# Optimization experiments

Hardware: AMD Instinct MI355X
Metric: run time of the kernel (lower is better)

The kernel has to match this reference:

```python
import jax, jax.numpy as jnp
import numpy as np

EPS = 1e-5  # BatchNorm eps; eval mode with running_mean=0, running_var=1

def _bn(x, g, b):
    return x * (g / jnp.sqrt(1.0 + EPS)) + b

def _lrelu(x):
    return jnp.where(x >= 0, x, 0.2 * x)

def setup_inputs() -> dict:
    key = jax.random.key(0)
    ks = jax.random.split(key, 30)
    def w(i, shape, s=0.05):
        return jax.random.normal(ks[i], shape, dtype=jnp.float32) * s
    inp = {"x": jax.random.normal(ks[0], (8, 10, 4096), dtype=jnp.float32), "k": 20}
    inp.update(
        w1=w(1, (64, 9)),    g1=1.0 + w(2, (64,), 0.1),  b1=w(3, (64,), 0.1),
        w2=w(4, (64, 64)),   g2=1.0 + w(5, (64,), 0.1),  b2=w(6, (64,), 0.1),
        w3=w(7, (128, 128)), g3=1.0 + w(8, (128,), 0.1), b3=w(9, (128,), 0.1),
        w4=w(10, (256, 128)), g4=1.0 + w(11, (256,), 0.1), b4=w(12, (256,), 0.1),
        w5=w(13, (1024, 256)), g5=1.0 + w(14, (1024,), 0.1), b5=w(15, (1024,), 0.1),
        l1w=w(16, (512, 1472)), l1b=w(17, (512,), 0.1),
        g6=1.0 + w(18, (512,), 0.1), b6=w(19, (512,), 0.1),
        l2w=w(20, (256, 512)), l2b=w(21, (256,), 0.1),
        g7=1.0 + w(22, (256,), 0.1), b7=w(23, (256,), 0.1),
        l3w=w(24, (2, 256)), l3b=w(25, (2,), 0.1),
    )
    return inp

def reference(x, k, w1, g1, b1, w2, g2, b2, w3, g3, b3, w4, g4, b4, w5, g5, b5,
              l1w, l1b, g6, b6, l2w, l2b, g7, b7, l3w, l3b):
    B, C, N = x.shape
    # --- kNN on xyz (first 3 channels); topk of negative squared distance ---
    xyz = x[:, :3, :]
    xx = jnp.sum(xyz * xyz, axis=1)                        # [B,N]
    inner = jnp.einsum('bcn,bcm->bnm', xyz, xyz)           # [B,N,N]
    pd = 2.0 * inner - xx[:, :, None] - xx[:, None, :]     # -||xi-xj||^2
    idx = jax.lax.top_k(pd, k)[1]                          # [B,N,k]
    # --- neighbor gather + edge features (xyz_i, rgb_i, rgb_i - rgb_j) ---
    xt = jnp.transpose(x, (0, 2, 1))                       # [B,N,C]
    nbr = xt[jnp.arange(B)[:, None, None], idx]            # [B,N,k,C]
    xyz_i = jnp.broadcast_to(xt[:, :, None, :3], (B, N, k, 3))
    rgb_i = jnp.broadcast_to(xt[:, :, None, 3:6], (B, N, k, 3))
    f = jnp.concatenate([xyz_i, rgb_i, rgb_i - nbr[..., 3:6]], axis=-1)  # [B,N,k,9]
    # --- EdgeConv MLPs (1x1 convs) + max over neighbors ---
    h = _lrelu(_bn(jnp.einsum('bnkc,oc->bnko', f, w1), g1, b1))
    h = _lrelu(_bn(jnp.einsum('bnkc,oc->bnko', h, w2), g2, b2))
    x1 = jnp.max(h, axis=2)                                # [B,N,64]
    x2 = _lrelu(_bn(jnp.einsum('bnc,oc->bno', jnp.concatenate([x1, x1], -1), w3), g3, b3))  # [B,N,128]
    x3 = _lrelu(_bn(jnp.einsum('bnc,oc->bno', x2, w4), g4, b4))  # [B,N,256]
    x4 = jnp.max(x3, axis=1)                               # [B,256] global max pool
    # conv5 applied to x4 repeated over N; max over identical copies == itself
    xg = _lrelu(_bn(x4 @ w5.T, g5, b5))                    # [B,1024]
    feat = jnp.concatenate([jnp.broadcast_to(xg[:, None, :], (B, N, 1024)), x3, x2, x1], axis=-1)  # [B,N,1472]
    h = _lrelu(_bn(feat @ l1w.T + l1b, g6, b6))            # dropout = identity (eval)
    h = _lrelu(_bn(h @ l2w.T + l2b, g7, b7))
    out = h @ l3w.T + l3b                                  # [B,N,num_classes]
    return jnp.transpose(out, (0, 2, 1))                   # [B,num_classes,N]
```

## Files before the change

### kernel.cpp

```cpp
#include <hip/hip_runtime.h>


#define KNN 20
#define NPID 32768
#define RS 0.99999500003750f

#define X3_PO 8388608
#define X2_PO 4194304
#define X1_PO 2097152

typedef unsigned short ushort_t;
typedef unsigned int u32;
typedef __attribute__((ext_vector_type(8))) short bf16x8;
typedef __attribute__((ext_vector_type(4))) float f32x4;

#define LDS_PTR(p) ((__attribute__((address_space(3))) void*)(p))
#define GLB_PTR(p) ((const __attribute__((address_space(1))) void*)(p))

__device__ __forceinline__ float lrelu(float z) { return z >= 0.f ? z : 0.2f * z; }
__device__ __forceinline__ unsigned short f2bf(float f) {
  unsigned int u = __float_as_uint(f);
  return (unsigned short)((u + 0x7fffu + ((u >> 16) & 1u)) >> 16);
}
__device__ __forceinline__ float bf2f(unsigned short h) { return __uint_as_float((unsigned int)h << 16); }
__device__ __forceinline__ u32 pack2(u32 e0, u32 e1) { return (e1 << 16) | (e0 & 0xffffu); }
__device__ __forceinline__ u32 encf(float f) {
  const u32 u = __float_as_uint(f);
  return (u >> 31) ? ~u : (u | 0x80000000u);
}
__device__ __forceinline__ float decf(u32 e) {
  return __uint_as_float((e >> 31) ? (e ^ 0x80000000u) : ~e);
}
__device__ __forceinline__ f32x4 mfma16(uint4 a, uint4 b, f32x4 c) {
  return __builtin_amdgcn_mfma_f32_16x16x32_bf16(
      __builtin_bit_cast(bf16x8, a), __builtin_bit_cast(bf16x8, b), c, 0, 0, 0);
}

__global__ __launch_bounds__(256) void xyzw_kernel(const float* __restrict__ x, float4* __restrict__ xyzw) {
  const int i = blockIdx.x * 256 + threadIdx.x;
  const int b = i >> 12, n = i & 4095;
  const float* xb = x + (size_t)b * 40960;
  const float px = xb[n], py = xb[4096 + n], pz = xb[8192 + n];
  const float xx = __fadd_rn(__fadd_rn(__fmul_rn(px, px), __fmul_rn(py, py)), __fmul_rn(pz, pz));
  float4 v; v.x = px; v.y = py; v.z = pz; v.w = xx;
  xyzw[i] = v;
}

__global__ __launch_bounds__(1024) void knn_kernel(const float4* __restrict__ xyzw, int* __restrict__ idxo) {
  __shared__ __align__(16) float4 pt[4096];
  __shared__ float cval[16][64];
  __shared__ int cidx[16][64];
  const int tid = threadIdx.x, lane = tid & 63, wave = tid >> 6;
  const int pid = blockIdx.x * 16 + wave;
  const int b = pid >> 12, n = pid & 4095;
  const float4* xw = xyzw + ((size_t)b << 12);
#pragma unroll
  for (int r = 0; r < 4; ++r) {
    const int chunk = wave * 4 + r;
    __builtin_amdgcn_global_load_lds(GLB_PTR(xw + chunk * 64 + lane),
                                     LDS_PTR((char*)pt + chunk * 1024), 16, 0, 0);
  }
  const float4 P = xw[n];
  const float px = P.x, py = P.y, pz = P.z, xxn = P.w;
  __syncthreads();
  float d[64];
  float lmax = -3.4e38f;
#pragma unroll
  for (int j = 0; j < 64; ++j) {
    const float4 Q = pt[j * 64 + lane];
    const float inner = __fadd_rn(__fadd_rn(__fmul_rn(px, Q.x), __fmul_rn(py, Q.y)), __fmul_rn(pz, Q.z));
    const float pd = __fsub_rn(__fsub_rn(__fmul_rn(2.0f, inner), xxn), Q.w);
    d[j] = pd;
    lmax = fmaxf(lmax, pd);
  }
  float v = lmax;
#pragma unroll
  for (int k = 2; k <= 64; k <<= 1) {
#pragma unroll
    for (int j = k >> 1; j > 0; j >>= 1) {
      const float ov = __shfl_xor(v, j, 64);
      const bool keepMax = (((lane & k) == 0) == ((lane & j) == 0));
      v = keepMax ? fmaxf(v, ov) : fminf(v, ov);
    }
  }
  const float t0 = __shfl(v, 19, 64);
  int base = 0;
#pragma unroll
  for (int j = 0; j < 64; ++j) {
    const bool take = (d[j] >= t0);
    const unsigned long long mk = __ballot(take);
    if (take) {
      const int pos = base + __popcll(mk & ((1ull << lane) - 1ull));
      if (pos < 64) {
        cval[wave][pos] = d[j];
        cidx[wave][pos] = (j << 6) + lane;
      }
    }
    base += (int)__popcll(mk);
  }
  const int C = base;
  int* out = idxo + (size_t)pid * KNN;
  if (C <= 64) {
    unsigned long long key = 0ull;
    if (lane < C) {
      const unsigned int u = __float_as_uint(cval[wave][lane]);
      const unsigned int ou = (u & 0x80000000u) ? ~u : (u | 0x80000000u);
      key = ((unsigned long long)ou << 32) | (unsigned long long)(0xFFFFFFFFu - (unsigned int)cidx[wave][lane]);
    }
#pragma unroll
    for (int k = 2; k <= 64; k <<= 1) {
#pragma unroll
      for (int j = k >> 1; j > 0; j >>= 1) {
        const unsigned long long ok = (unsigned long long)__shfl_xor((long long)key, j, 64);
        const bool keepMax = (((lane & k) == 0) == ((lane & j) == 0));
        const bool gt = key > ok;
        key = (keepMax == gt) ? key : ok;
      }
    }
    if (lane < KNN) out[lane] = (int)(0xFFFFFFFFu - (unsigned int)key);
  } else {
    unsigned long long used = 0ull;
#pragma unroll 1
    for (int it = 0; it < KNN; ++it) {
      float lv = -3.4e38f;
      int li = 1 << 30;
#pragma unroll
      for (int j = 0; j < 64; ++j) {
        if (!((used >> j) & 1ull) && d[j] > lv) {
          lv = d[j];
          li = (j << 6) + lane;
        }
      }
      float bv = lv;
      int bi = li;
#pragma unroll
      for (int s = 1; s < 64; s <<= 1) {
        const float ovv = __shfl_xor(bv, s, 64);
        const int oii = __shfl_xor(bi, s, 64);
        if (ovv > bv || (ovv == bv && oii < bi)) { bv = ovv; bi = oii; }
      }
      if (lane == 0) out[it] = bi;
      if ((bi & 63) == lane) used |= 1ull << (bi >> 6);
    }
  }
}

__global__ __launch_bounds__(256) void edge_kernel(const float* __restrict__ x, const int* __restrict__ idxi,
    const float* __restrict__ w1, const float* __restrict__ g1, const float* __restrict__ b1,
    const ushort_t* __restrict__ w2p, const float* __restrict__ g2, const float* __restrict__ b2,
    ushort_t* __restrict__ x1o) {
  __shared__ u32 hstage[4][16][64];
  const int tid = threadIdx.x, lane = tid & 63, wave = tid >> 6;
  const int fr = lane & 15, kg = lane >> 4;
  const int pbase = blockIdx.x * 64 + wave * 16;
  const int b = (blockIdx.x * 64) >> 12;
  const float* xq = x + (size_t)b * 40960;

  const int nA = (pbase + fr) & 4095;
  float cv[6]; ushort_t chv[6], clv[6];
#pragma unroll
  for (int j = 0; j < 6; ++j) {
    cv[j] = xq[j * 4096 + nA];
    chv[j] = f2bf(cv[j]);
    clv[j] = f2bf(cv[j] - bf2f(chv[j]));
  }
  const float crv = cv[3], cgv = cv[4], cbv = cv[5];

  u32 aC0 = 0, aC1 = 0, aC2 = 0, aC3 = 0;
  if (kg == 0) { aC0 = pack2(chv[0], chv[1]); aC1 = pack2(chv[2], chv[3]); aC2 = pack2(chv[4], chv[5]); }
  else if (kg == 1) { aC0 = (u32)chv[0] << 16; aC1 = pack2(chv[1], chv[2]); aC2 = pack2(chv[3], chv[4]); aC3 = chv[5]; }
  else if (kg == 2) { aC1 = pack2(clv[0], clv[1]); aC2 = pack2(clv[2], clv[3]); aC3 = pack2(clv[4], clv[5]); }

  float s1v[4], t1v[4], s2v[4], t2v[4];
#pragma unroll
  for (int fj = 0; fj < 4; ++fj) {
    const int och = fj * 16 + fr;
    s1v[fj] = g1[och] * RS; t1v[fj] = b1[och];
    s2v[fj] = g2[och] * RS; t2v[fj] = b2[och];
  }

  uint4 w1Bv[4];
#pragma unroll
  for (int fj = 0; fj < 4; ++fj) {
    const int och = fj * 16 + fr;
    ushort_t wh[9], wl[9];
#pragma unroll
    for (int j = 0; j < 9; ++j) {
      const float wv = w1[och * 9 + j];
      wh[j] = f2bf(wv);
      wl[j] = f2bf(wv - bf2f(wh[j]));
    }
    uint4 q;
    if (kg == 0)      { q.x = pack2(wh[0], wh[1]); q.y = pack2(wh[2], wh[3]); q.z = pack2(wh[4], wh[5]); q.w = pack2(wh[6], wh[7]); }
    else if (kg == 1) { q.x = pack2(wh[8], wl[0]); q.y = pack2(wl[1], wl[2]); q.z = pack2(wl[3], wl[4]); q.w = pack2(wl[5], wl[6]); }
    else if (kg == 2) { q.x = pack2(wl[7], wl[8]); q.y = pack2(wh[0], wh[1]); q.z = pack2(wh[2], wh[3]); q.w = pack2(wh[4], wh[5]); }
    else              { q.x = pack2(wh[6], wh[7]); q.y = pack2(wh[8], 0);     q.z = 0;                   q.w = 0; }
    w1Bv[fj] = q;
  }

  uint4 w2Bh[4][2], w2Bl[4][2];
#pragma unroll
  for (int fj = 0; fj < 4; ++fj) {
    const int och = fj * 16 + fr;
#pragma unroll
    for (int sub = 0; sub < 2; ++sub) {
      const ushort_t* ph = w2p + och * 64 + sub * 32 + kg * 8;
      w2Bh[fj][sub] = *(const uint4*)ph;
      w2Bl[fj][sub] = *(const uint4*)(ph + 4096);
    }
  }

  const int prow = (pbase + fr) * KNN;
  int miA = idxi[prow];
  int miN = idxi[prow + 1];
  float pr = xq[12288 + miA], pg = xq[16384 + miA], pb = xq[20480 + miA];

  f32x4 xm[4];
#pragma unroll
  for (int fj = 0; fj < 4; ++fj) { xm[fj][0] = -3.4e38f; xm[fj][1] = -3.4e38f; xm[fj][2] = -3.4e38f; xm[fj][3] = -3.4e38f; }
  const f32x4 zz = {0.f, 0.f, 0.f, 0.f};

#pragma unroll 1
  for (int kk = 0; kk < KNN; ++kk) {
    const float nrv = pr, ngv = pg, nbv = pb;
    if (kk < KNN - 1) { pr = xq[12288 + miN]; pg = xq[16384 + miN]; pb = xq[20480 + miN]; }
    if (kk < KNN - 2) { miN = idxi[prow + kk + 2]; }

    const float dr = crv - nrv, dg = cgv - ngv, db = cbv - nbv;
    const ushort_t drh = f2bf(dr), dgh = f2bf(dg), dbh = f2bf(db);
    const ushort_t drl = f2bf(dr - bf2f(drh)), dgl = f2bf(dg - bf2f(dgh)), dbl = f2bf(db - bf2f(dbh));

    uint4 aF;
    if (kg == 0)      { aF.x = aC0; aF.y = aC1; aF.z = aC2; aF.w = pack2(drh, dgh); }
    else if (kg == 1) { aF.x = aC0 | dbh; aF.y = aC1; aF.z = aC2; aF.w = aC3 | ((u32)drh << 16); }
    else if (kg == 2) { aF.x = pack2(dgh, dbh); aF.y = aC1; aF.z = aC2; aF.w = aC3; }
    else              { aF.x = pack2(drl, dgl); aF.y = (u32)dbl; aF.z = 0; aF.w = 0; }

    f32x4 h1a[4];
#pragma unroll
    for (int fj = 0; fj < 4; ++fj) h1a[fj] = mfma16(aF, w1Bv[fj], zz);

#pragma unroll
    for (int fj = 0; fj < 4; ++fj)
#pragma unroll
      for (int r = 0; r < 4; ++r) {
        float z = h1a[fj][r] * s1v[fj] + t1v[fj];
        z = fmaxf(z, 0.2f * z);
        const ushort_t hi = f2bf(z), lo = f2bf(z - bf2f(hi));
        const int pC = kg * 4 + r;
        hstage[wave][pC][(fj * 16 + fr) ^ ((pC & 7) << 3)] = ((u32)hi << 16) | lo;
      }

    f32x4 a2[4] = {zz, zz, zz, zz};
#pragma unroll
    for (int sub = 0; sub < 2; ++sub) {
      const u32* rp = &hstage[wave][fr][(sub * 32 + kg * 8) ^ ((fr & 7) << 3)];
      const uint4 q0 = *(const uint4*)rp;
      const uint4 q1 = *(const uint4*)(rp + 4);
      uint4 ah, al;
      ah.x = __builtin_amdgcn_perm(q0.y, q0.x, 0x07060302u); al.x = __builtin_amdgcn_perm(q0.y, q0.x, 0x05040100u);
      ah.y = __builtin_amdgcn_perm(q0.w, q0.z, 0x07060302u); al.y = __builtin_amdgcn_perm(q0.w, q0.z, 0x05040100u);
      ah.z = __builtin_amdgcn_perm(q1.y, q1.x, 0x07060302u); al.z = __builtin_amdgcn_perm(q1.y, q1.x, 0x05040100u);
      ah.w = __builtin_amdgcn_perm(q1.w, q1.z, 0x07060302u); al.w = __builtin_amdgcn_perm(q1.w, q1.z, 0x05040100u);
#pragma unroll
      for (int fj = 0; fj < 4; ++fj) {
        a2[fj] = mfma16(ah, w2Bh[fj][sub], a2[fj]);
        a2[fj] = mfma16(ah, w2Bl[fj][sub], a2[fj]);
        a2[fj] = mfma16(al, w2Bh[fj][sub], a2[fj]);
      }
    }

#pragma unroll
    for (int fj = 0; fj < 4; ++fj)
#pragma unroll
      for (int r = 0; r < 4; ++r) {
        float z = a2[fj][r] * s2v[fj] + t2v[fj];
        z = fmaxf(z, 0.2f * z);
        xm[fj][r] = fmaxf(xm[fj][r], z);
      }
  }

#pragma unroll
  for (int fj = 0; fj < 4; ++fj)
#pragma unroll
    for (int r = 0; r < 4; ++r) {
      const size_t e = (size_t)(pbase + kg * 4 + r) * 64 + fj * 16 + fr;
      const float v = xm[fj][r];
      const ushort_t hi = f2bf(v);
      x1o[e] = hi;
      x1o[X1_PO + e] = f2bf(v - bf2f(hi));
    }
}

__global__ __launch_bounds__(256) void prep_kernel(const float* __restrict__ w3, const float* __restrict__ w4,
    const float* __restrict__ l1w, const float* __restrict__ l2w, const float* __restrict__ w2,
    ushort_t* __restrict__ w3fp, ushort_t* __restrict__ w4p,
    ushort_t* __restrict__ l1wp, ushort_t* __restrict__ l2wp, ushort_t* __restrict__ w2p,
    u32* __restrict__ x4u) {
  const int i = blockIdx.x * 256 + threadIdx.x;
  float f; ushort_t* hp; int n, j;
  if (i < 8192) {
    const int o = i >> 6, c = i & 63;
    f = w3[o * 128 + c] + w3[o * 128 + 64 + c];
    hp = w3fp; n = 8192; j = i;
  } else if (i < 8192 + 32768) {
    j = i - 8192; f = w4[j]; hp = w4p; n = 32768;
  } else if (i < 8192 + 32768 + 131072) {
    j = i - 8192 - 32768; f = l2w[j]; hp = l2wp; n = 131072;
  } else if (i < 172032 + 229376) {
    j = i - 172032;
    const int row = j / 448, col = j - row * 448;
    f = l1w[row * 1472 + 1024 + col];
    hp = l1wp; n = 229376;
  } else if (i < 401408 + 4096) {
    j = i - 401408; f = w2[j]; hp = w2p; n = 4096;
  } else if (i < 405504 + 2048) {
    x4u[i - 405504] = 0u;
    return;
  } else return;
  const unsigned short h = f2bf(f);
  hp[j] = h;
  hp[n + j] = f2bf(f - bf2f(h));
}

template <int MODE, int OUTF32, int DOMAX>
__global__ __launch_bounds__(256) void gemm_bf16(
    const ushort_t* __restrict__ A, const ushort_t* __restrict__ W, void* __restrict__ outv,
    const int Ktot, const int Nout, const int n_tiles,
    const int aPO, const int wPO, const int outPO,
    const float* __restrict__ gg, const float* __restrict__ bb,
    const float* __restrict__ linb, const int do_lrelu,
    const float* __restrict__ ybp, const ushort_t* __restrict__ x3,
    const ushort_t* __restrict__ x2, const ushort_t* __restrict__ x1,
    u32* __restrict__ x4u) {
  __shared__ __align__(16) ushort_t lds[16384];
  const int tid = threadIdx.x, lane = tid & 63, wid = tid >> 6;
  const int nwg = gridDim.x;
  int id = (blockIdx.x & 7) * (nwg >> 3) + (blockIdx.x >> 3);
  const int mt = id / n_tiles, nt = id - mt * n_tiles;
  const int m0 = mt * 128, o0 = nt * 128;
  const int fr = lane & 15, kg = lane >> 4;
  const int wr = wid >> 1, wc = wid & 1;
  int rA[4], rB[4];
#pragma unroll
  for (int i = 0; i < 4; ++i) { rA[i] = wr * 64 + i * 16 + fr; rB[i] = wc * 64 + i * 16 + fr; }
  f32x4 acc[4][4] = {};
  const ushort_t* srcB = (wid == 2) ? W : W + wPO;
  const ushort_t* srcA0 = (MODE == 0) ? ((wid == 0) ? A : A + aPO) : nullptr;
  const int pl = (wid == 1);

  for (int kc = 0; kc < Ktot; kc += 32) {
#pragma unroll
    for (int c = 0; c < 8; ++c) {
      const int row = c * 16 + (lane >> 2);
      const int rslot = (lane & 3) ^ ((row >> 1) & 3);
      const int k = kc + rslot * 8;
      const ushort_t* q;
      if (wid >= 2) {
        q = srcB + (size_t)(o0 + row) * Ktot + k;
      } else if (MODE == 0) {
        q = srcA0 + (size_t)(m0 + row) * Ktot + k;
      } else {
        const int m = m0 + row;
        if (k < 256)      q = x3 + pl * X3_PO + (size_t)m * 256 + k;
        else if (k < 384) q = x2 + pl * X2_PO + (size_t)m * 128 + (k - 256);
        else              q = x1 + pl * X1_PO + (size_t)m * 64 + (k - 384);
      }
      __builtin_amdgcn_global_load_lds(GLB_PTR(q), LDS_PTR(&lds[wid * 4096 + c * 512]), 16, 0, 0);
    }
    __syncthreads();
    bf16x8 ah[4], al[4], bh[4], bl[4];
#pragma unroll
    for (int i = 0; i < 4; ++i) {
      const int off = rA[i] * 32 + ((kg ^ ((rA[i] >> 1) & 3)) << 3);
      ah[i] = *(const bf16x8*)&lds[off];
      al[i] = *(const bf16x8*)&lds[4096 + off];
    }
#pragma unroll
    for (int j = 0; j < 4; ++j) {
      const int off = rB[j] * 32 + ((kg ^ ((rB[j] >> 1) & 3)) << 3);
      bh[j] = *(const bf16x8*)&lds[8192 + off];
      bl[j] = *(const bf16x8*)&lds[12288 + off];
    }
#pragma unroll
    for (int i = 0; i < 4; ++i)
#pragma unroll
      for (int j = 0; j < 4; ++j) {
        acc[i][j] = __builtin_amdgcn_mfma_f32_16x16x32_bf16(ah[i], bh[j], acc[i][j], 0, 0, 0);
        acc[i][j] = __builtin_amdgcn_mfma_f32_16x16x32_bf16(ah[i], bl[j], acc[i][j], 0, 0, 0);
        acc[i][j] = __builtin_amdgcn_mfma_f32_16x16x32_bf16(al[i], bh[j], acc[i][j], 0, 0, 0);
      }
    __syncthreads();
  }
  float s[4], t[4];
#pragma unroll
  for (int j = 0; j < 4; ++j) {
    const int o = o0 + wc * 64 + j * 16 + fr;
    s[j] = gg[o] * RS;
    float add = linb ? linb[o] : 0.f;
    if (MODE == 1) add += ybp[((m0 >> 12) << 9) + o];
    t[j] = bb[o] + add * s[j];
  }
  float cm[4] = {-3.4e38f, -3.4e38f, -3.4e38f, -3.4e38f};
#pragma unroll
  for (int i = 0; i < 4; ++i) {
#pragma unroll
    for (int j = 0; j < 4; ++j) {
      const int col = o0 + wc * 64 + j * 16 + fr;
#pragma unroll
      for (int r = 0; r < 4; ++r) {
        const int row = m0 + wr * 64 + i * 16 + kg * 4 + r;
        float z = acc[i][j][r] * s[j] + t[j];
        if (do_lrelu) z = lrelu(z);
        if (DOMAX) cm[j] = fmaxf(cm[j], z);
        if (OUTF32) {
          ((float*)outv)[(size_t)row * Nout + col] = z;
        } else {
          ushort_t* oh = (ushort_t*)outv;
          const unsigned short h = f2bf(z);
          oh[(size_t)row * Nout + col] = h;
          oh[outPO + (size_t)row * Nout + col] = f2bf(z - bf2f(h));
        }
      }
    }
  }
  if (DOMAX) {
    __syncthreads();
    u32* mcol = (u32*)lds;
    if (tid < 128) mcol[tid] = 0u;
    __syncthreads();
#pragma unroll
    for (int j = 0; j < 4; ++j) atomicMax(&mcol[wc * 64 + j * 16 + fr], encf(cm[j]));
    __syncthreads();
    if (tid < 128) atomicMax(&x4u[((m0 >> 12) << 8) + o0 + tid], mcol[tid]);
  }
}

__global__ __launch_bounds__(256) void xg_kernel(const u32* __restrict__ x4u, const float* __restrict__ w5,
    const float* __restrict__ g5, const float* __restrict__ b5, float* __restrict__ xgf) {
  const int lane = threadIdx.x & 63, wave = threadIdx.x >> 6;
  const int o = blockIdx.x * 4 + wave;
  const int b = o >> 10, oc = o & 1023;
  const uint4 xu = *(const uint4*)&x4u[b * 256 + lane * 4];
  const float4 w = *(const float4*)&w5[(size_t)oc * 256 + lane * 4];
  float acc = decf(xu.x) * w.x + decf(xu.y) * w.y + decf(xu.z) * w.z + decf(xu.w) * w.w;
#pragma unroll
  for (int s = 1; s < 64; s <<= 1) acc += __shfl_xor(acc, s, 64);
  if (lane == 0) xgf[o] = lrelu(acc * (g5[oc] * RS) + b5[oc]);
}

__global__ __launch_bounds__(256) void yb_kernel(const float* __restrict__ xgf, const float* __restrict__ l1w,
    float* __restrict__ yb) {
  const int lane = threadIdx.x & 63, wave = threadIdx.x >> 6;
  const int o = blockIdx.x * 4 + wave;
  const int b = o >> 9, oc = o & 511;
  float acc = 0.f;
#pragma unroll
  for (int i = 0; i < 4; ++i) {
    const int k = i * 256 + lane * 4;
    const float4 w = *(const float4*)&l1w[(size_t)oc * 1472 + k];
    const float4 g = *(const float4*)&xgf[b * 1024 + k];
    acc += w.x * g.x + w.y * g.y + w.z * g.z + w.w * g.w;
  }
#pragma unroll
  for (int s = 1; s < 64; s <<= 1) acc += __shfl_xor(acc, s, 64);
  if (lane == 0) yb[o] = acc;
}

__global__ __launch_bounds__(256) void l3_kernel(const float* __restrict__ h6, const float* __restrict__ l3w,
    const float* __restrict__ l3b, float* __restrict__ out) {
  __shared__ float wl[512];
  const int tid = threadIdx.x;
  wl[tid] = l3w[tid]; wl[256 + tid] = l3w[256 + tid];
  __syncthreads();
  const int m = blockIdx.x * 256 + tid;
  float a0 = 0.f, a1 = 0.f;
#pragma unroll
  for (int c = 0; c < 256; c += 4) {
    const float4 h = *(const float4*)(h6 + (size_t)m * 256 + c);
    a0 += h.x * wl[c] + h.y * wl[c + 1] + h.z * wl[c + 2] + h.w * wl[c + 3];
    a1 += h.x * wl[256 + c] + h.y * wl[256 + c + 1] + h.z * wl[256 + c + 2] + h.w * wl[256 + c + 3];
  }
  const int b = m >> 12, n = m & 4095;
  out[(size_t)b * 8192 + n] = a0 + l3b[0];
  out[(size_t)b * 8192 + 4096 + n] = a1 + l3b[1];
}

extern "C" void kernel_launch(void* const* d_in, const int* in_sizes, int n_in,
                              void* d_out, int out_size, void* d_ws, size_t ws_size,
                              hipStream_t stream) {
  const float* x   = (const float*)d_in[0];
  const float* w1  = (const float*)d_in[2];
  const float* g1  = (const float*)d_in[3];
  const float* b1  = (const float*)d_in[4];
  const float* w2  = (const float*)d_in[5];
  const float* g2  = (const float*)d_in[6];
  const float* b2  = (const float*)d_in[7];
  const float* w3  = (const float*)d_in[8];
  const float* g3  = (const float*)d_in[9];
  const float* b3  = (const float*)d_in[10];
  const float* w4  = (const float*)d_in[11];
  const float* g4  = (const float*)d_in[12];
  const float* b4  = (const float*)d_in[13];
  const float* w5  = (const float*)d_in[14];
  const float* g5  = (const float*)d_in[15];
  const float* b5  = (const float*)d_in[16];
  const float* l1w = (const float*)d_in[17];
  const float* l1b = (const float*)d_in[18];
  const float* g6  = (const float*)d_in[19];
  const float* b6  = (const float*)d_in[20];
  const float* l2w = (const float*)d_in[21];
  const float* l2b = (const float*)d_in[22];
  const float* g7  = (const float*)d_in[23];
  const float* b7  = (const float*)d_in[24];
  const float* l3w = (const float*)d_in[25];
  const float* l3b = (const float*)d_in[26];
  float* outp = (float*)d_out;

  char* ws = (char*)d_ws;
  int*      idx  = (int*)(ws + 0);
  ushort_t* x1   = (ushort_t*)(ws + 2621440);
  ushort_t* x2   = (ushort_t*)(ws + 11010048);
  ushort_t* x3   = (ushort_t*)(ws + 27787264);
  ushort_t* w2p  = (ushort_t*)(ws + 61341696);
  u32*      x4u  = (u32*)(ws + 61358080);
  float*    xgf  = (float*)(ws + 61407232);
  float*    ybp  = (float*)(ws + 61448192);
  ushort_t* w3fp = (ushort_t*)(ws + 61440000);
  ushort_t* w4p  = (ushort_t*)(ws + 61472768);
  ushort_t* l2wp = (ushort_t*)(ws + 61603840);
  ushort_t* l1wp = (ushort_t*)(ws + 62128128);
  ushort_t* h5   = (ushort_t*)(ws + 65142784);
  float4*   xyzw = (float4*)(ws + 132251648);
  float*    h6   = (float*)(ws + 11010048);

  xyzw_kernel<<<128, 256, 0, stream>>>(x, xyzw);
  knn_kernel<<<NPID / 16, 1024, 0, stream>>>(xyzw, idx);
  prep_kernel<<<1592, 256, 0, stream>>>(w3, w4, l1w, l2w, w2, w3fp, w4p, l1wp, l2wp, w2p, x4u);
  edge_kernel<<<NPID / 64, 256, 0, stream>>>(x, idx, w1, g1, b1, w2p, g2, b2, x1);
  gemm_bf16<0, 0, 0><<<256, 256, 0, stream>>>(x1, w3fp, x2, 64, 128, 1, X1_PO, 8192, X2_PO,
                                              g3, b3, nullptr, 1, nullptr, nullptr, nullptr, nullptr, nullptr);
  gemm_bf16<0, 0, 1><<<512, 256, 0, stream>>>(x2, w4p, x3, 128, 256, 2, X2_PO, 32768, X3_PO,
                                              g4, b4, nullptr, 1, nullptr, nullptr, nullptr, nullptr, x4u);
  xg_kernel<<<2048, 256, 0, stream>>>(x4u, w5, g5, b5, xgf);
  yb_kernel<<<1024, 256, 0, stream>>>(xgf, l1w, ybp);
  gemm_bf16<1, 0, 0><<<1024, 256, 0, stream>>>(nullptr, l1wp, h5, 448, 512, 4, 0, 229376, 16777216,
                                               g6, b6, l1b, 1, ybp, x3, x2, x1, nullptr);
  gemm_bf16<0, 1, 0><<<512, 256, 0, stream>>>(h5, l2wp, h6, 512, 256, 2, 16777216, 131072, 0,
                                              g7, b7, l2b, 1, nullptr, nullptr, nullptr, nullptr, nullptr);
  l3_kernel<<<128, 256, 0, stream>>>(h6, l3w, l3b, outp);
}
```

Measured before the change: 259.2 us.

## Process two queries per wave in kNN with smaller blocks and half-tile LDS staging

Each wave in the kNN kernel now handles two query points, so every candidate point loaded from LDS is reused for two distance computations. Blocks shrink from 1024 to 256 threads, and the point cloud is staged through LDS in two 2048-point halves to cut shared memory per block. When both queries have at most 32 candidates, the final sort packs both queries into one 32-wide bitonic network across the wave. This doubles the per-thread distance registers (float2[64]), which can lower occupancy, and adds a second barrier phase.

```diff
diff --git a/kernel.cpp b/kernel.cpp
--- a/kernel.cpp
+++ b/kernel.cpp
@@ -46,101 +46,145 @@
   xyzw[i] = v;
 }
 
-__global__ __launch_bounds__(1024) void knn_kernel(const float4* __restrict__ xyzw, int* __restrict__ idxo) {
-  __shared__ __align__(16) float4 pt[4096];
-  __shared__ float cval[16][64];
-  __shared__ int cidx[16][64];
+__global__ __launch_bounds__(256, 3) void knn_kernel(const float4* __restrict__ xyzw, int* __restrict__ idxo) {
+  __shared__ __align__(16) float4 pt[2048];
+  __shared__ float cval[8][64];
+  __shared__ int cidx[8][64];
   const int tid = threadIdx.x, lane = tid & 63, wave = tid >> 6;
-  const int pid = blockIdx.x * 16 + wave;
-  const int b = pid >> 12, n = pid & 4095;
+  const int qbase = blockIdx.x * 8 + wave * 2;
+  const int b = qbase >> 12;
   const float4* xw = xyzw + ((size_t)b << 12);
-#pragma unroll
-  for (int r = 0; r < 4; ++r) {
-    const int chunk = wave * 4 + r;
-    __builtin_amdgcn_global_load_lds(GLB_PTR(xw + chunk * 64 + lane),
-                                     LDS_PTR((char*)pt + chunk * 1024), 16, 0, 0);
-  }
-  const float4 P = xw[n];
-  const float px = P.x, py = P.y, pz = P.z, xxn = P.w;
-  __syncthreads();
-  float d[64];
-  float lmax = -3.4e38f;
-#pragma unroll
-  for (int j = 0; j < 64; ++j) {
-    const float4 Q = pt[j * 64 + lane];
-    const float inner = __fadd_rn(__fadd_rn(__fmul_rn(px, Q.x), __fmul_rn(py, Q.y)), __fmul_rn(pz, Q.z));
-    const float pd = __fsub_rn(__fsub_rn(__fmul_rn(2.0f, inner), xxn), Q.w);
-    d[j] = pd;
-    lmax = fmaxf(lmax, pd);
-  }
-  float v = lmax;
-#pragma unroll
-  for (int k = 2; k <= 64; k <<= 1) {
-#pragma unroll
-    for (int j = k >> 1; j > 0; j >>= 1) {
-      const float ov = __shfl_xor(v, j, 64);
-      const bool keepMax = (((lane & k) == 0) == ((lane & j) == 0));
-      v = keepMax ? fmaxf(v, ov) : fminf(v, ov);
-    }
-  }
-  const float t0 = __shfl(v, 19, 64);
-  int base = 0;
-#pragma unroll
-  for (int j = 0; j < 64; ++j) {
-    const bool take = (d[j] >= t0);
-    const unsigned long long mk = __ballot(take);
-    if (take) {
-      const int pos = base + __popcll(mk & ((1ull << lane) - 1ull));
-      if (pos < 64) {
-        cval[wave][pos] = d[j];
-        cidx[wave][pos] = (j << 6) + lane;
-      }
-    }
-    base += (int)__popcll(mk);
-  }
-  const int C = base;
-  int* out = idxo + (size_t)pid * KNN;
-  if (C <= 64) {
+  const int nA = qbase & 4095;
+  const float4 PA = xw[nA];
+  const float4 PB = xw[nA + 1];
+  float2 d[64];
+  float lmaxA = -3.4e38f, lmaxB = -3.4e38f;
+#pragma unroll
+  for (int t = 0; t < 2; ++t) {
+    if (t) __syncthreads();
+#pragma unroll
+    for (int r = 0; r < 8; ++r) {
+      const int chunk = wave * 8 + r;
+      __builtin_amdgcn_global_load_lds(GLB_PTR(xw + t * 2048 + chunk * 64 + lane),
+                                       LDS_PTR((char*)pt + chunk * 1024), 16, 0, 0);
+    }
+    __syncthreads();
+#pragma unroll
+    for (int jj = 0; jj < 32; ++jj) {
+      const float4 Q = pt[jj * 64 + lane];
+      const float iA = __fadd_rn(__fadd_rn(__fmul_rn(PA.x, Q.x), __fmul_rn(PA.y, Q.y)), __fmul_rn(PA.z, Q.z));
+      const float pdA = __fsub_rn(__fsub_rn(__fmul_rn(2.0f, iA), PA.w), Q.w);
+      const float iB = __fadd_rn(__fadd_rn(__fmul_rn(PB.x, Q.x), __fmul_rn(PB.y, Q.y)), __fmul_rn(PB.z, Q.z));
+      const float pdB = __fsub_rn(__fsub_rn(__fmul_rn(2.0f, iB), PB.w), Q.w);
+      d[t * 32 + jj].x = pdA;
+      d[t * 32 + jj].y = pdB;
+      lmaxA = fmaxf(lmaxA, pdA);
+      lmaxB = fmaxf(lmaxB, pdB);
+    }
+  }
+  float t0q[2];
+#pragma unroll
+  for (int q = 0; q < 2; ++q) {
+    float v = q ? lmaxB : lmaxA;
+#pragma unroll
+    for (int k = 2; k <= 64; k <<= 1) {
+#pragma unroll
+      for (int j = k >> 1; j > 0; j >>= 1) {
+        const float ov = __shfl_xor(v, j, 64);
+        const bool keepMax = (((lane & k) == 0) == ((lane & j) == 0));
+        v = keepMax ? fmaxf(v, ov) : fminf(v, ov);
+      }
+    }
+    t0q[q] = __shfl(v, 19, 64);
+  }
+  int Cq[2];
+#pragma unroll
+  for (int q = 0; q < 2; ++q) {
+    const float t0 = t0q[q];
+    int base = 0;
+#pragma unroll
+    for (int j = 0; j < 64; ++j) {
+      const float dv = q ? d[j].y : d[j].x;
+      const bool take = (dv >= t0);
+      const unsigned long long mk = __ballot(take);
+      if (take) {
+        const int pos = base + __popcll(mk & ((1ull << lane) - 1ull));
+        if (pos < 64) {
+          cval[wave * 2 + q][pos] = dv;
+          cidx[wave * 2 + q][pos] = (j << 6) + lane;
+        }
+      }
+      base += (int)__popcll(mk);
+    }
+    Cq[q] = base;
+  }
+  int* outA = idxo + (size_t)qbase * KNN;
+  if (Cq[0] <= 32 && Cq[1] <= 32) {
+    const int qsel = lane >> 5, c = lane & 31;
+    const int row = wave * 2 + qsel;
+    const int Cc = qsel ? Cq[1] : Cq[0];
     unsigned long long key = 0ull;
-    if (lane < C) {
-      const unsigned int u = __float_as_uint(cval[wave][lane]);
-      const unsigned int ou = (u & 0x80000000u) ? ~u : (u | 0x80000000u);
-      key = ((unsigned long long)ou << 32) | (unsigned long long)(0xFFFFFFFFu - (unsigned int)cidx[wave][lane]);
-    }
-#pragma unroll
-    for (int k = 2; k <= 64; k <<= 1) {
+    if (c < Cc) {
+      key = ((unsigned long long)encf(cval[row][c]) << 32) |
+            (unsigned long long)(0xFFFFFFFFu - (unsigned int)cidx[row][c]);
+    }
+#pragma unroll
+    for (int k = 2; k <= 32; k <<= 1) {
 #pragma unroll
       for (int j = k >> 1; j > 0; j >>= 1) {
         const unsigned long long ok = (unsigned long long)__shfl_xor((long long)key, j, 64);
-        const bool keepMax = (((lane & k) == 0) == ((lane & j) == 0));
-        const bool gt = key > ok;
-        key = (keepMax == gt) ? key : ok;
-      }
-    }
-    if (lane < KNN) out[lane] = (int)(0xFFFFFFFFu - (unsigned int)key);
+        const bool keepMax = (((c & k) == 0) == ((c & j) == 0));
+        key = (keepMax == (key > ok)) ? key : ok;
+      }
+    }
+    if (c < KNN) outA[qsel * KNN + c] = (int)(0xFFFFFFFFu - (unsigned int)key);
   } else {
-    unsigned long long used = 0ull;
+#pragma unroll
+    for (int q = 0; q < 2; ++q) {
+      int* out = outA + q * KNN;
+      const int C = Cq[q];
+      if (C <= 64) {
+        unsigned long long key = 0ull;
+        if (lane < C) {
+          key = ((unsigned long long)encf(cval[wave * 2 + q][lane]) << 32) |
+                (unsigned long long)(0xFFFFFFFFu - (unsigned int)cidx[wave * 2 + q][lane]);
+        }
+#pragma unroll
+        for (int k = 2; k <= 64; k <<= 1) {
+#pragma unroll
+          for (int j = k >> 1; j > 0; j >>= 1) {
+            const unsigned long long ok = (unsigned long long)__shfl_xor((long long)key, j, 64);
+            const bool keepMax = (((lane & k) == 0) == ((lane & j) == 0));
+            key = (keepMax == (key > ok)) ? key : ok;
+          }
+        }
+        if (lane < KNN) out[lane] = (int)(0xFFFFFFFFu - (unsigned int)key);
+      } else {
+        unsigned long long used = 0ull;
 #pragma unroll 1
-    for (int it = 0; it < KNN; ++it) {
-      float lv = -3.4e38f;
-      int li = 1 << 30;
-#pragma unroll
-      for (int j = 0; j < 64; ++j) {
-        if (!((used >> j) & 1ull) && d[j] > lv) {
-          lv = d[j];
-          li = (j << 6) + lane;
+        for (int it = 0; it < KNN; ++it) {
+          float lv = -3.4e38f;
+          int li = 1 << 30;
+#pragma unroll
+          for (int j = 0; j < 64; ++j) {
+            const float dv = q ? d[j].y : d[j].x;
+            if (!((used >> j) & 1ull) && dv > lv) {
+              lv = dv;
+              li = (j << 6) + lane;
+            }
+          }
+          float bv = lv;
+          int bi = li;
+#pragma unroll
+          for (int s = 1; s < 64; s <<= 1) {
+            const float ovv = __shfl_xor(bv, s, 64);
+            const int oii = __shfl_xor(bi, s, 64);
+            if (ovv > bv || (ovv == bv && oii < bi)) { bv = ovv; bi = oii; }
+          }
+          if (lane == 0) out[it] = bi;
+          if ((bi & 63) == lane) used |= 1ull << (bi >> 6);
         }
       }
-      float bv = lv;
-      int bi = li;
-#pragma unroll
-      for (int s = 1; s < 64; s <<= 1) {
-        const float ovv = __shfl_xor(bv, s, 64);
-        const int oii = __shfl_xor(bi, s, 64);
-        if (ovv > bv || (ovv == bv && oii < bi)) { bv = ovv; bi = oii; }
-      }
-      if (lane == 0) out[it] = bi;
-      if ((bi & 63) == lane) used |= 1ull << (bi >> 6);
     }
   }
 }
@@ -535,7 +579,7 @@
   float*    h6   = (float*)(ws + 11010048);
 
   xyzw_kernel<<<128, 256, 0, stream>>>(x, xyzw);
-  knn_kernel<<<NPID / 16, 1024, 0, stream>>>(xyzw, idx);
+  knn_kernel<<<NPID / 8, 256, 0, stream>>>(xyzw, idx);
   prep_kernel<<<1592, 256, 0, stream>>>(w3, w4, l1w, l2w, w2, w3fp, w4p, l1wp, l2wp, w2p, x4u);
   edge_kernel<<<NPID / 64, 256, 0, stream>>>(x, idx, w1, g1, b1, w2p, g2, b2, x1);
   gemm_bf16<0, 0, 0><<<256, 256, 0, stream>>>(x1, w3fp, x2, 64, 128, 1, X1_PO, 8192, X2_PO,
```

After: 250.8 us. -3.2%, faster.
